# Kernel optimization log

Measured on AMD Instinct MI355X. Metric: run time of the kernel, lower is better.

## Reference

```python
import jax, jax.numpy as jnp
import numpy as np

B, S, D_IN, H, K = 1024, 256, 64, 256, 64

def setup_inputs() -> dict:
    key = jax.random.key(0)
    ks = jax.random.split(key, 11)
    s = lambda k, shape, fan_in: jax.random.uniform(k, shape, jnp.float32, -1.0, 1.0) / np.sqrt(fan_in)
    return {
        "input_seq": jax.random.normal(ks[0], (B, S, D_IN), jnp.float32),
        "W_emb": s(ks[1], (D_IN, H), D_IN), "b_emb": s(ks[2], (H,), D_IN),
        "W_k": s(ks[3], (H, K), H), "b_k": s(ks[4], (K,), H),
        "W_q": s(ks[5], (H, K), H), "b_q": s(ks[6], (K,), H),
        "W_v": s(ks[7], (H, H), H), "b_v": s(ks[8], (H,), H),
        "W_d": s(ks[9], (S * H, 1), S * H), "b_d": s(ks[10], (1,), S * H),
    }

def reference(input_seq, W_emb, b_emb, W_k, b_k, W_q, b_q, W_v, b_v, W_d, b_d):
    # embedded: (B, S, H)
    embedded = input_seq @ W_emb + b_emb
    # keys softmax over sequence dim (dim=1), shape (B, S, K)
    keys = jax.nn.softmax(embedded @ W_k + b_k, axis=1)
    queries = embedded @ W_q + b_q           # (B, S, K)
    values = embedded @ W_v + b_v            # (B, S, H)
    # context_lambda = keys^T @ values: (B, K, H)
    context = jnp.einsum('bsk,bsh->bkh', keys, values)
    # attention_map = queries @ context: (B, S, H)
    attn = jnp.einsum('bsk,bkh->bsh', queries, context)
    flat = attn.reshape(-1, S * H)           # (B, S*H)
    return flat @ W_d + b_d                  # (B, 1)
```

## Files before the change

kernel.cpp:

```cpp
#include <hip/hip_runtime.h>
#include <hip/hip_bf16.h>

typedef _Float16 half8 __attribute__((ext_vector_type(8)));
typedef _Float16 half4 __attribute__((ext_vector_type(4)));
typedef float    f32x4 __attribute__((ext_vector_type(4)));

constexpr int Bb = 1024;
constexpr int TS = 512;

constexpr int W_WEV  = 0;
constexpr int W_MTH  = 65536;
constexpr int W_WEKH = 98304;
constexpr int W_WEQH = 106496;
constexpr int W_BEQ  = 114688;
constexpr int W_BEV  = 114944;
constexpr int W_CS   = 115968;
constexpr int W_CB   = 116992;
constexpr int W_MS   = 118016;
constexpr int W_C0   = 118272;

__global__ void pre1_kernel(const float* __restrict__ W_emb, const float* __restrict__ b_emb,
                            const float* __restrict__ W_k,   const float* __restrict__ W_q,
                            const float* __restrict__ b_q,   const float* __restrict__ W_v,
                            const float* __restrict__ b_v,   const float* __restrict__ W_d,
                            char* __restrict__ wsb) {
  int i = blockIdx.x * blockDim.x + threadIdx.x;
  if (i < 16384) {
    int d = i >> 8, h = i & 255;
    float a = 0.f;
#pragma unroll 8
    for (int hp = 0; hp < 256; ++hp) a += W_emb[d*256 + hp] * W_v[hp*256 + h];
    ((float*)(wsb + W_WEV))[i] = a;
  } else if (i < 20480) {
    int j = i - 16384; int k = j & 63, d = j >> 6;
    float a = 0.f;
#pragma unroll 8
    for (int h = 0; h < 256; ++h) a += W_emb[d*256 + h] * W_k[h*64 + k];
    ((_Float16*)(wsb + W_WEKH))[k*64 + d] = (_Float16)a;
  } else if (i < 24576) {
    int j = i - 20480; int k = j & 63, d = j >> 6;
    float a = 0.f;
#pragma unroll 8
    for (int h = 0; h < 256; ++h) a += W_emb[d*256 + h] * W_q[h*64 + k];
    ((_Float16*)(wsb + W_WEQH))[k*64 + d] = (_Float16)a;
  } else if (i < 24640) {
    int k = i - 24576;
    float a = b_q[k];
    for (int h = 0; h < 256; ++h) a += b_emb[h] * W_q[h*64 + k];
    ((float*)(wsb + W_BEQ))[k] = a;
  } else if (i < 24896) {
    int h = i - 24640;
    float a = b_v[h];
    for (int hp = 0; hp < 256; ++hp) a += b_emb[hp] * W_v[hp*256 + h];
    ((float*)(wsb + W_BEV))[h] = a;
  } else if (i < 25152) {
    int h = i - 24896;
    float a = 0.f;
    for (int s = 0; s < 256; ++s) a += W_d[s*256 + h];
    ((float*)(wsb + W_CS))[h] = a;
  }
}

__global__ void pre2_kernel(const float* __restrict__ W_d, const float* __restrict__ b_d,
                            char* __restrict__ wsb) {
  int i = blockIdx.x * blockDim.x + threadIdx.x;
  const float* wev = (const float*)(wsb + W_WEV);
  if (i < 16384) {
    int d = i >> 8, s = i & 255;
    float a = 0.f;
#pragma unroll 8
    for (int h = 0; h < 256; ++h) a += W_d[s*256 + h] * wev[d*256 + h];
    ((_Float16*)(wsb + W_MTH))[i] = (_Float16)a;
  } else if (i < 16640) {
    int s = i - 16384;
    const float* bev = (const float*)(wsb + W_BEV);
    float a = 0.f;
    for (int h = 0; h < 256; ++h) a += W_d[s*256 + h] * bev[h];
    ((float*)(wsb + W_CB))[s] = a;
  } else if (i < 16704) {
    int d = i - 16640;
    const float* cs = (const float*)(wsb + W_CS);
    float a = 0.f;
    for (int h = 0; h < 256; ++h) a += wev[d*256 + h] * cs[h];
    ((float*)(wsb + W_MS))[d] = a;
  } else if (i == 16704) {
    const float* cs  = (const float*)(wsb + W_CS);
    const float* bev = (const float*)(wsb + W_BEV);
    const float* beq = (const float*)(wsb + W_BEQ);
    float cbsum = 0.f;
    for (int h = 0; h < 256; ++h) cbsum += cs[h] * bev[h];
    float bqsum = 0.f;
    for (int k = 0; k < 64; ++k) bqsum += beq[k];
    ((float*)(wsb + W_C0))[0] = b_d[0] + cbsum * bqsum;
  }
}

__device__ __forceinline__ int adrA(int s, int d) {
  return ((s << 7) + (d << 1)) ^ ((s & 7) << 4);
}
__device__ __forceinline__ int adrR(int r, int c) {
  return 32768 + (((r << 9) + (c << 1)) ^ ((r & 7) << 4));
}
__device__ __forceinline__ int adrU(int k, int d) {
  return 65536 + (((k << 7) + (d << 1)) ^ ((k & 7) << 4));
}

#define MFMA16(A, B, C) __builtin_amdgcn_mfma_f32_16x16x32_f16((A), (B), (C), 0, 0, 0)

__global__ __launch_bounds__(TS, 4) void main_kernel(const float* __restrict__ inp_g,
                                                     const char* __restrict__ wsb,
                                                     float* __restrict__ out) {
  __shared__ __align__(16) char smem[73728];
  __shared__ __align__(16) float s_scr[776];

  const int b = blockIdx.x, t = threadIdx.x;
  const int l = t & 63, w = t >> 6;
  const int lhi = l >> 4, llo = l & 15;

  const float* inp = inp_g + (size_t)b * 16384;

#pragma unroll
  for (int it = 0; it < 8; ++it) {
    int i = t + it * TS;
    int s = i >> 4, dq = i & 15;
    float4 v = ((const float4*)inp)[i];
    half4 h;
    h[0] = (_Float16)v.x; h[1] = (_Float16)v.y;
    h[2] = (_Float16)v.z; h[3] = (_Float16)v.w;
    *(half4*)(smem + adrA(s, dq * 4)) = h;
  }
  __syncthreads();

  f32x4 zero4 = {0.f, 0.f, 0.f, 0.f};
  f32x4 clg[2][4], cq[2][4];
#pragma unroll
  for (int tl = 0; tl < 2; ++tl)
#pragma unroll
    for (int n = 0; n < 4; ++n) { clg[tl][n] = zero4; cq[tl][n] = zero4; }
  {
    const _Float16* wekh = (const _Float16*)(wsb + W_WEKH);
    const _Float16* weqh = (const _Float16*)(wsb + W_WEQH);
    const int srowA = w * 32 + llo, srowB = srowA + 16;
#pragma unroll
    for (int ks = 0; ks < 2; ++ks) {
      const int kd = ks * 32 + lhi * 8;
      half8 Aa = *(const half8*)(smem + adrA(srowA, kd));
      half8 Ab = *(const half8*)(smem + adrA(srowB, kd));
      half8 Bk[4];
#pragma unroll
      for (int n = 0; n < 4; ++n) Bk[n] = *(const half8*)(wekh + (n * 16 + llo) * 64 + kd);
#pragma unroll
      for (int n = 0; n < 4; ++n) {
        clg[0][n] = MFMA16(Aa, Bk[n], clg[0][n]);
        clg[1][n] = MFMA16(Ab, Bk[n], clg[1][n]);
      }
      half8 Bq[4];
#pragma unroll
      for (int n = 0; n < 4; ++n) Bq[n] = *(const half8*)(weqh + (n * 16 + llo) * 64 + kd);
#pragma unroll
      for (int n = 0; n < 4; ++n) {
        cq[0][n] = MFMA16(Aa, Bq[n], cq[0][n]);
        cq[1][n] = MFMA16(Ab, Bq[n], cq[1][n]);
      }
    }
  }

  float e[2][4][4];
  float acc = 0.f;
  const int d0 = (w & 3) * 16;
  const int ka = (w >> 2) * 16, kb = ka + 32;
  half8 Bm[8];
  {
#pragma unroll
    for (int tl = 0; tl < 2; ++tl) {
      int sbase = w * 32 + tl * 16 + lhi * 4;
#pragma unroll
      for (int n = 0; n < 4; ++n) {
        half4 qh;
#pragma unroll
        for (int r = 0; r < 4; ++r) qh[r] = (_Float16)cq[tl][n][r];
        *(half4*)(smem + adrR(n * 16 + llo, sbase)) = qh;
      }
    }
    const float* cb = (const float*)(wsb + W_CB);
#pragma unroll
    for (int tl = 0; tl < 2; ++tl)
#pragma unroll
      for (int r = 0; r < 4; ++r) {
        float qs = (cq[tl][0][r] + cq[tl][1][r]) + (cq[tl][2][r] + cq[tl][3][r]);
        acc += cb[w * 32 + tl * 16 + lhi * 4 + r] * qs;
      }
    const _Float16* mth = (const _Float16*)(wsb + W_MTH);
#pragma unroll
    for (int j = 0; j < 8; ++j) Bm[j] = *(const half8*)(mth + (d0 + llo) * 256 + j * 32 + lhi * 8);
#pragma unroll
    for (int n = 0; n < 4; ++n) {
      float sum = 0.f;
#pragma unroll
      for (int tl = 0; tl < 2; ++tl)
#pragma unroll
        for (int r = 0; r < 4; ++r) { e[tl][n][r] = __expf(clg[tl][n][r]); sum += e[tl][n][r]; }
      sum += __shfl_xor(sum, 16);
      sum += __shfl_xor(sum, 32);
      if (lhi == 0) s_scr[(n * 16 + llo) * 12 + w] = sum;
    }
  }
  __syncthreads();

#pragma unroll
  for (int n = 0; n < 4; ++n) {
    const float4* cp = (const float4*)(s_scr + (n * 16 + llo) * 12);
    float4 c0 = cp[0], c1 = cp[1];
    float ss = ((c0.x + c0.y) + (c0.z + c0.w)) + ((c1.x + c1.y) + (c1.z + c1.w));
    float rs = __builtin_amdgcn_rcpf(ss);
#pragma unroll
    for (int tl = 0; tl < 2; ++tl)
#pragma unroll
      for (int r = 0; r < 4; ++r) e[tl][n][r] *= rs;
  }

  {
    f32x4 cta = zero4, ctb = zero4;
#pragma unroll
    for (int ks = 0; ks < 8; ++ks) {
      const int kd = ks * 32 + lhi * 8;
      half8 Aqa = *(const half8*)(smem + adrR(ka + llo, kd));
      half8 Aqb = *(const half8*)(smem + adrR(kb + llo, kd));
      cta = MFMA16(Aqa, Bm[ks], cta);
      ctb = MFMA16(Aqb, Bm[ks], ctb);
    }
    const float* beq = (const float*)(wsb + W_BEQ);
    const float* msv = (const float*)(wsb + W_MS);
    float msd = msv[d0 + llo];
#pragma unroll
    for (int r = 0; r < 4; ++r) {
      float Uva = cta[r] + beq[ka + lhi * 4 + r] * msd;
      *(_Float16*)(smem + adrU(ka + lhi * 4 + r, d0 + llo)) = (_Float16)Uva;
      float Uvb = ctb[r] + beq[kb + lhi * 4 + r] * msd;
      *(_Float16*)(smem + adrU(kb + lhi * 4 + r, d0 + llo)) = (_Float16)Uvb;
    }
  }
  __syncthreads();

  {
    const int srowA = w * 32 + llo, srowB = srowA + 16;
    f32x4 cga[4], cgb[4];
#pragma unroll
    for (int n = 0; n < 4; ++n) { cga[n] = zero4; cgb[n] = zero4; }
#pragma unroll
    for (int ks = 0; ks < 2; ++ks) {
      const int kd = ks * 32 + lhi * 8;
      half8 Aa = *(const half8*)(smem + adrA(srowA, kd));
      half8 Ab = *(const half8*)(smem + adrA(srowB, kd));
      half8 Bu[4];
#pragma unroll
      for (int n = 0; n < 4; ++n) Bu[n] = *(const half8*)(smem + adrU(n * 16 + llo, kd));
#pragma unroll
      for (int n = 0; n < 4; ++n) {
        cga[n] = MFMA16(Aa, Bu[n], cga[n]);
        cgb[n] = MFMA16(Ab, Bu[n], cgb[n]);
      }
    }
#pragma unroll
    for (int n = 0; n < 4; ++n) {
      float dot = 0.f;
#pragma unroll
      for (int r = 0; r < 4; ++r)
        dot += e[0][n][r] * cga[n][r] + e[1][n][r] * cgb[n][r];
      acc += dot;
    }
  }

#pragma unroll
  for (int off = 32; off; off >>= 1) acc += __shfl_down(acc, off);
  if (l == 0) s_scr[768 + w] = acc;
  __syncthreads();
  if (t == 0) {
    float tot = ((const float*)(wsb + W_C0))[0];
#pragma unroll
    for (int g = 0; g < 8; ++g) tot += s_scr[768 + g];
    out[b] = tot;
  }
}

extern "C" void kernel_launch(void* const* d_in, const int* in_sizes, int n_in,
                              void* d_out, int out_size, void* d_ws, size_t ws_size,
                              hipStream_t stream) {
  (void)in_sizes; (void)n_in; (void)out_size; (void)ws_size;
  const float* input_seq = (const float*)d_in[0];
  const float* W_emb = (const float*)d_in[1];
  const float* b_emb = (const float*)d_in[2];
  const float* W_k   = (const float*)d_in[3];
  const float* W_q   = (const float*)d_in[5];
  const float* b_q   = (const float*)d_in[6];
  const float* W_v   = (const float*)d_in[7];
  const float* b_v   = (const float*)d_in[8];
  const float* W_d   = (const float*)d_in[9];
  const float* b_d   = (const float*)d_in[10];
  char* wsb  = (char*)d_ws;
  float* out = (float*)d_out;

  pre1_kernel<<<(25152 + 255) / 256, 256, 0, stream>>>(
      W_emb, b_emb, W_k, W_q, b_q, W_v, b_v, W_d, wsb);
  pre2_kernel<<<(16705 + 255) / 256, 256, 0, stream>>>(W_d, b_d, wsb);
  main_kernel<<<Bb, TS, 0, stream>>>(input_seq, wsb, out);
}
```

Before: 61.93 us.

## Keep input A-fragments in registers, drop LDS staging, shrink shared memory

Each wave now loads its input rows straight from global memory into half8 MFMA A-fragments held in registers for the whole kernel. This removes the 32 KB LDS input buffer and one barrier. Softmax exponentials are stored as packed fp16, and normalisation is deferred to the final dot product, cutting register use. Shared memory shrinks to about 43 KB and launch bounds are raised to 6 blocks per CU to gain occupancy. The risks are uncoalesced global loads, register pressure under the tighter bound, and fp16 rounding of the exp values.

```diff
diff --git a/kernel.cpp b/kernel.cpp
--- a/kernel.cpp
+++ b/kernel.cpp
@@ -3,6 +3,7 @@
 
 typedef _Float16 half8 __attribute__((ext_vector_type(8)));
 typedef _Float16 half4 __attribute__((ext_vector_type(4)));
+typedef _Float16 half2v __attribute__((ext_vector_type(2)));
 typedef float    f32x4 __attribute__((ext_vector_type(4)));
 
 constexpr int Bb = 1024;
@@ -95,23 +96,20 @@
   }
 }
 
-__device__ __forceinline__ int adrA(int s, int d) {
-  return ((s << 7) + (d << 1)) ^ ((s & 7) << 4);
-}
 __device__ __forceinline__ int adrR(int r, int c) {
-  return 32768 + (((r << 9) + (c << 1)) ^ ((r & 7) << 4));
+  return (((r << 9) + (c << 1)) ^ ((r & 7) << 4));
 }
 __device__ __forceinline__ int adrU(int k, int d) {
-  return 65536 + (((k << 7) + (d << 1)) ^ ((k & 7) << 4));
+  return 32768 + (((k << 7) + (d << 1)) ^ ((k & 7) << 4));
 }
 
 #define MFMA16(A, B, C) __builtin_amdgcn_mfma_f32_16x16x32_f16((A), (B), (C), 0, 0, 0)
 
-__global__ __launch_bounds__(TS, 4) void main_kernel(const float* __restrict__ inp_g,
+__global__ __launch_bounds__(TS, 6) void main_kernel(const float* __restrict__ inp_g,
                                                      const char* __restrict__ wsb,
                                                      float* __restrict__ out) {
-  __shared__ __align__(16) char smem[73728];
-  __shared__ __align__(16) float s_scr[776];
+  __shared__ __align__(16) char smem[43136];
+  float* scrf = (float*)(smem + 40960);
 
   const int b = blockIdx.x, t = threadIdx.x;
   const int l = t & 63, w = t >> 6;
@@ -119,105 +117,116 @@
 
   const float* inp = inp_g + (size_t)b * 16384;
 
-#pragma unroll
-  for (int it = 0; it < 8; ++it) {
-    int i = t + it * TS;
-    int s = i >> 4, dq = i & 15;
-    float4 v = ((const float4*)inp)[i];
-    half4 h;
-    h[0] = (_Float16)v.x; h[1] = (_Float16)v.y;
-    h[2] = (_Float16)v.z; h[3] = (_Float16)v.w;
-    *(half4*)(smem + adrA(s, dq * 4)) = h;
-  }
-  __syncthreads();
+  half8 Af[4];
+  {
+    const int srA = w * 32 + llo;
+#pragma unroll
+    for (int tl = 0; tl < 2; ++tl)
+#pragma unroll
+      for (int ks = 0; ks < 2; ++ks) {
+        const float4* p = (const float4*)(inp + (srA + tl * 16) * 64 + ks * 32 + lhi * 8);
+        float4 v0 = p[0], v1 = p[1];
+        half8 h;
+        h[0] = (_Float16)v0.x; h[1] = (_Float16)v0.y; h[2] = (_Float16)v0.z; h[3] = (_Float16)v0.w;
+        h[4] = (_Float16)v1.x; h[5] = (_Float16)v1.y; h[6] = (_Float16)v1.z; h[7] = (_Float16)v1.w;
+        Af[tl * 2 + ks] = h;
+      }
+  }
 
   f32x4 zero4 = {0.f, 0.f, 0.f, 0.f};
-  f32x4 clg[2][4], cq[2][4];
-#pragma unroll
-  for (int tl = 0; tl < 2; ++tl)
-#pragma unroll
-    for (int n = 0; n < 4; ++n) { clg[tl][n] = zero4; cq[tl][n] = zero4; }
-  {
+  float acc = 0.f;
+  half2v ep[2][4][2];
+
+  {
+    f32x4 clg[2][4];
+#pragma unroll
+    for (int tl = 0; tl < 2; ++tl)
+#pragma unroll
+      for (int n = 0; n < 4; ++n) clg[tl][n] = zero4;
     const _Float16* wekh = (const _Float16*)(wsb + W_WEKH);
-    const _Float16* weqh = (const _Float16*)(wsb + W_WEQH);
-    const int srowA = w * 32 + llo, srowB = srowA + 16;
 #pragma unroll
     for (int ks = 0; ks < 2; ++ks) {
       const int kd = ks * 32 + lhi * 8;
-      half8 Aa = *(const half8*)(smem + adrA(srowA, kd));
-      half8 Ab = *(const half8*)(smem + adrA(srowB, kd));
       half8 Bk[4];
 #pragma unroll
       for (int n = 0; n < 4; ++n) Bk[n] = *(const half8*)(wekh + (n * 16 + llo) * 64 + kd);
 #pragma unroll
       for (int n = 0; n < 4; ++n) {
-        clg[0][n] = MFMA16(Aa, Bk[n], clg[0][n]);
-        clg[1][n] = MFMA16(Ab, Bk[n], clg[1][n]);
-      }
+        clg[0][n] = MFMA16(Af[ks],     Bk[n], clg[0][n]);
+        clg[1][n] = MFMA16(Af[2 + ks], Bk[n], clg[1][n]);
+      }
+    }
+#pragma unroll
+    for (int n = 0; n < 4; ++n) {
+      float sum = 0.f;
+      float ev[2][4];
+#pragma unroll
+      for (int tl = 0; tl < 2; ++tl)
+#pragma unroll
+        for (int r = 0; r < 4; ++r) { ev[tl][r] = __expf(clg[tl][n][r]); sum += ev[tl][r]; }
+#pragma unroll
+      for (int tl = 0; tl < 2; ++tl) {
+        half2v p0, p1;
+        p0[0] = (_Float16)ev[tl][0]; p0[1] = (_Float16)ev[tl][1];
+        p1[0] = (_Float16)ev[tl][2]; p1[1] = (_Float16)ev[tl][3];
+        ep[tl][n][0] = p0; ep[tl][n][1] = p1;
+      }
+      sum += __shfl_xor(sum, 16);
+      sum += __shfl_xor(sum, 32);
+      if (lhi == 0) scrf[(n * 16 + llo) * 8 + w] = sum;
+    }
+  }
+
+  {
+    f32x4 cq[2][4];
+#pragma unroll
+    for (int tl = 0; tl < 2; ++tl)
+#pragma unroll
+      for (int n = 0; n < 4; ++n) cq[tl][n] = zero4;
+    const _Float16* weqh = (const _Float16*)(wsb + W_WEQH);
+#pragma unroll
+    for (int ks = 0; ks < 2; ++ks) {
+      const int kd = ks * 32 + lhi * 8;
       half8 Bq[4];
 #pragma unroll
       for (int n = 0; n < 4; ++n) Bq[n] = *(const half8*)(weqh + (n * 16 + llo) * 64 + kd);
 #pragma unroll
       for (int n = 0; n < 4; ++n) {
-        cq[0][n] = MFMA16(Aa, Bq[n], cq[0][n]);
-        cq[1][n] = MFMA16(Ab, Bq[n], cq[1][n]);
-      }
-    }
-  }
-
-  float e[2][4][4];
-  float acc = 0.f;
+        cq[0][n] = MFMA16(Af[ks],     Bq[n], cq[0][n]);
+        cq[1][n] = MFMA16(Af[2 + ks], Bq[n], cq[1][n]);
+      }
+    }
+#pragma unroll
+    for (int tl = 0; tl < 2; ++tl) {
+      int sbase = w * 32 + tl * 16 + lhi * 4;
+#pragma unroll
+      for (int n = 0; n < 4; ++n) {
+        half4 qh;
+#pragma unroll
+        for (int r = 0; r < 4; ++r) qh[r] = (_Float16)cq[tl][n][r];
+        *(half4*)(smem + adrR(n * 16 + llo, sbase)) = qh;
+      }
+    }
+    const float* cb = (const float*)(wsb + W_CB);
+#pragma unroll
+    for (int tl = 0; tl < 2; ++tl)
+#pragma unroll
+      for (int r = 0; r < 4; ++r) {
+        float qs = (cq[tl][0][r] + cq[tl][1][r]) + (cq[tl][2][r] + cq[tl][3][r]);
+        acc += cb[w * 32 + tl * 16 + lhi * 4 + r] * qs;
+      }
+  }
+
   const int d0 = (w & 3) * 16;
   const int ka = (w >> 2) * 16, kb = ka + 32;
   half8 Bm[8];
   {
-#pragma unroll
-    for (int tl = 0; tl < 2; ++tl) {
-      int sbase = w * 32 + tl * 16 + lhi * 4;
-#pragma unroll
-      for (int n = 0; n < 4; ++n) {
-        half4 qh;
-#pragma unroll
-        for (int r = 0; r < 4; ++r) qh[r] = (_Float16)cq[tl][n][r];
-        *(half4*)(smem + adrR(n * 16 + llo, sbase)) = qh;
-      }
-    }
-    const float* cb = (const float*)(wsb + W_CB);
-#pragma unroll
-    for (int tl = 0; tl < 2; ++tl)
-#pragma unroll
-      for (int r = 0; r < 4; ++r) {
-        float qs = (cq[tl][0][r] + cq[tl][1][r]) + (cq[tl][2][r] + cq[tl][3][r]);
-        acc += cb[w * 32 + tl * 16 + lhi * 4 + r] * qs;
-      }
     const _Float16* mth = (const _Float16*)(wsb + W_MTH);
 #pragma unroll
-    for (int j = 0; j < 8; ++j) Bm[j] = *(const half8*)(mth + (d0 + llo) * 256 + j * 32 + lhi * 8);
-#pragma unroll
-    for (int n = 0; n < 4; ++n) {
-      float sum = 0.f;
-#pragma unroll
-      for (int tl = 0; tl < 2; ++tl)
-#pragma unroll
-        for (int r = 0; r < 4; ++r) { e[tl][n][r] = __expf(clg[tl][n][r]); sum += e[tl][n][r]; }
-      sum += __shfl_xor(sum, 16);
-      sum += __shfl_xor(sum, 32);
-      if (lhi == 0) s_scr[(n * 16 + llo) * 12 + w] = sum;
-    }
+    for (int j = 0; j < 8; ++j)
+      Bm[j] = *(const half8*)(mth + (d0 + llo) * 256 + j * 32 + lhi * 8);
   }
   __syncthreads();
-
-#pragma unroll
-  for (int n = 0; n < 4; ++n) {
-    const float4* cp = (const float4*)(s_scr + (n * 16 + llo) * 12);
-    float4 c0 = cp[0], c1 = cp[1];
-    float ss = ((c0.x + c0.y) + (c0.z + c0.w)) + ((c1.x + c1.y) + (c1.z + c1.w));
-    float rs = __builtin_amdgcn_rcpf(ss);
-#pragma unroll
-    for (int tl = 0; tl < 2; ++tl)
-#pragma unroll
-      for (int r = 0; r < 4; ++r) e[tl][n][r] *= rs;
-  }
 
   {
     f32x4 cta = zero4, ctb = zero4;
@@ -243,42 +252,46 @@
   __syncthreads();
 
   {
-    const int srowA = w * 32 + llo, srowB = srowA + 16;
     f32x4 cga[4], cgb[4];
 #pragma unroll
     for (int n = 0; n < 4; ++n) { cga[n] = zero4; cgb[n] = zero4; }
 #pragma unroll
     for (int ks = 0; ks < 2; ++ks) {
       const int kd = ks * 32 + lhi * 8;
-      half8 Aa = *(const half8*)(smem + adrA(srowA, kd));
-      half8 Ab = *(const half8*)(smem + adrA(srowB, kd));
       half8 Bu[4];
 #pragma unroll
       for (int n = 0; n < 4; ++n) Bu[n] = *(const half8*)(smem + adrU(n * 16 + llo, kd));
 #pragma unroll
       for (int n = 0; n < 4; ++n) {
-        cga[n] = MFMA16(Aa, Bu[n], cga[n]);
-        cgb[n] = MFMA16(Ab, Bu[n], cgb[n]);
+        cga[n] = MFMA16(Af[ks],     Bu[n], cga[n]);
+        cgb[n] = MFMA16(Af[2 + ks], Bu[n], cgb[n]);
       }
     }
 #pragma unroll
     for (int n = 0; n < 4; ++n) {
+      const float4* cp = (const float4*)(scrf + (n * 16 + llo) * 8);
+      float4 c0v = cp[0], c1v = cp[1];
+      float ss = ((c0v.x + c0v.y) + (c0v.z + c0v.w)) + ((c1v.x + c1v.y) + (c1v.z + c1v.w));
+      float rs = __builtin_amdgcn_rcpf(ss);
       float dot = 0.f;
 #pragma unroll
-      for (int r = 0; r < 4; ++r)
-        dot += e[0][n][r] * cga[n][r] + e[1][n][r] * cgb[n][r];
-      acc += dot;
+      for (int r = 0; r < 4; ++r) {
+        float ea = (float)ep[0][n][r >> 1][r & 1];
+        float eb = (float)ep[1][n][r >> 1][r & 1];
+        dot += ea * cga[n][r] + eb * cgb[n][r];
+      }
+      acc += dot * rs;
     }
   }
 
 #pragma unroll
   for (int off = 32; off; off >>= 1) acc += __shfl_down(acc, off);
-  if (l == 0) s_scr[768 + w] = acc;
+  if (l == 0) scrf[512 + w] = acc;
   __syncthreads();
   if (t == 0) {
     float tot = ((const float*)(wsb + W_C0))[0];
 #pragma unroll
-    for (int g = 0; g < 8; ++g) tot += s_scr[768 + g];
+    for (int g = 0; g < 8; ++g) tot += scrf[512 + g];
     out[b] = tot;
   }
 }
```

Measured after the change: 86.12 us. 1.39x slower.
